# Optimization experiments

Hardware: AMD Instinct MI355X
Metric: run time of the kernel (lower is better)

Reference implementation:

```python
import jax, jax.numpy as jnp
import numpy as np

B, S, D = 1, 2048, 1024
NH, NKV, WS = 8, 2, 64
HD = D // NH  # 128
E, HDIM, TOPK = 16, 512, 2
FP16_MIN = -65504.0
EPS = 1e-6
AUX_COEFF = 1e-5


def rmsnorm(x, w):
    return x * jax.lax.rsqrt(jnp.mean(x * x, axis=-1, keepdims=True) + EPS) * w


def setup_inputs() -> dict:
    key = jax.random.key(0)
    ks = jax.random.split(key, 24)
    r = lambda k, shape, fan: jax.random.normal(k, shape, dtype=jnp.float32) * (1.0 / np.sqrt(fan))
    return {
        "x": jax.random.normal(ks[0], (B, S, D), dtype=jnp.float32),
        "norm1_w": jnp.ones((D,), jnp.float32),
        "wq": r(ks[1], (D, NH * HD), D), "bq": jnp.zeros((NH * HD,), jnp.float32),
        "wk": r(ks[2], (D, NKV * HD), D), "bk": jnp.zeros((NKV * HD,), jnp.float32),
        "wv": r(ks[3], (D, NKV * HD), D), "bv": jnp.zeros((NKV * HD,), jnp.float32),
        "wo": r(ks[4], (NH * HD, D), NH * HD), "bo": jnp.zeros((D,), jnp.float32),
        "sink_bias": jnp.zeros((), jnp.float32),
        "norm2_w": jnp.ones((D,), jnp.float32),
        "router_w": r(ks[5], (D, E), D), "router_b": jnp.zeros((E,), jnp.float32),
        "w1": r(ks[6], (E, D, HDIM), D), "b1": jnp.zeros((E, HDIM), jnp.float32),
        "w2": r(ks[7], (E, HDIM, D), HDIM), "b2": jnp.zeros((E, D), jnp.float32),
    }


def reference(x, norm1_w, wq, bq, wk, bk, wv, bv, wo, bo, sink_bias,
              norm2_w, router_w, router_b, w1, b1, w2, b2):
    # ---- sliding-window attention with sink softmax ----
    h = rmsnorm(x, norm1_w)
    q = (h @ wq + bq).reshape(B, S, NH, HD).transpose(0, 2, 1, 3)    # [B,NH,S,HD]
    k = (h @ wk + bk).reshape(B, S, NKV, HD).transpose(0, 2, 1, 3)   # [B,NKV,S,HD]
    v = (h @ wv + bv).reshape(B, S, NKV, HD).transpose(0, 2, 1, 3)
    k = jnp.repeat(k, NH // NKV, axis=1)  # GQA expand -> [B,NH,S,HD]
    v = jnp.repeat(v, NH // NKV, axis=1)
    scores = jnp.einsum('bhqd,bhkd->bhqk', q, k) / np.sqrt(HD)
    i = jnp.arange(S)[:, None]
    j = jnp.arange(S)[None, :]
    band = (i - j >= 0) & (i - j <= WS - 1)  # causal sliding window
    scores = jnp.where(band, scores, FP16_MIN)
    m = jnp.maximum(jnp.max(scores, axis=-1, keepdims=True), sink_bias)
    ew = jnp.exp(scores - m)
    denom = jnp.sum(ew, axis=-1, keepdims=True) + jnp.exp(sink_bias - m)
    attn = ew / denom
    out = jnp.einsum('bhqk,bhkd->bhqd', attn, v).transpose(0, 2, 1, 3).reshape(B, S, D)
    x = x + (out @ wo + bo)

    # ---- MoE FFN ----
    h2 = rmsnorm(x, norm2_w)
    xf = h2.reshape(-1, D)                                  # [N,D]
    logits = (xf @ router_w + router_b) / 0.1               # [N,E]
    top_v, top_i = jax.lax.top_k(logits, TOPK)              # [N,k]
    top_w = jax.nn.softmax(top_v, axis=-1)
    probs = jax.nn.softmax(logits, axis=-1)
    aux_loss = jnp.sum(jnp.sum(probs, axis=0) ** 2) / E * AUX_COEFF
    # combine weights per (token, expert)
    gate = jnp.sum(jax.nn.one_hot(top_i, E, dtype=xf.dtype) * top_w[..., None], axis=1)  # [N,E]
    hmid = jax.nn.silu(jnp.einsum('nd,edh->neh', xf, w1) + b1)   # [N,E,H]
    y = jnp.einsum('neh,ehd->ned', hmid, w2) + b2                # [N,E,D]
    ffn = jnp.einsum('ne,ned->nd', gate, y)
    x = x + ffn.reshape(B, S, D)
    return x, aux_loss
```

## Files before the change

kernel.cpp:

```cpp
#include <hip/hip_runtime.h>
#include <hip/hip_bf16.h>

#define S     2048
#define D     1024
#define NH    8
#define NKV   2
#define HD    128
#define WS_   64
#define E_    16
#define HDIM  512
#define TOPK  2
#define NTOK  S
#define NSLOT (S*TOPK)
#define QKV_M (D + 2*NKV*HD)
#define KOFF  D
#define VOFF  (D + NKV*HD)
#define QB    8
#define WROWS (QB + WS_ - 1)
#define KPITCH 73
#define VPADF  132

typedef __attribute__((ext_vector_type(8))) short bf16x8;
typedef __attribute__((ext_vector_type(4))) float floatx4;

__device__ inline short f2bf(float f) {
    __hip_bfloat16 b = __float2bfloat16(f);
    return *reinterpret_cast<short*>(&b);
}

__global__ __launch_bounds__(256) void tconv_all(
    const float* __restrict__ wq, const float* __restrict__ wk,
    const float* __restrict__ wv, const float* __restrict__ wo,
    const float* __restrict__ w1, const float* __restrict__ w2,
    const float* __restrict__ bq, const float* __restrict__ bk,
    const float* __restrict__ bv, const float* __restrict__ router_w,
    short* __restrict__ wqkvT, short* __restrict__ woT,
    short* __restrict__ w1T, short* __restrict__ w2T,
    float* __restrict__ bqkv, float* __restrict__ rwT,
    const float* __restrict__ x, const float* __restrict__ norm1_w,
    short* __restrict__ h_bf, float* __restrict__ gcsum,
    int* __restrict__ ghist)
{
    int id = blockIdx.x;
    if (id >= 18983) {
        int row = id - 18983, t = threadIdx.x;
        float4 v = ((const float4*)(x + (size_t)row * D))[t];
        float ss = v.x*v.x + v.y*v.y + v.z*v.z + v.w*v.w;
        #pragma unroll
        for (int off = 32; off; off >>= 1) ss += __shfl_xor(ss, off, 64);
        __shared__ float red[4];
        if ((t & 63) == 0) red[t >> 6] = ss;
        __syncthreads();
        float total = red[0] + red[1] + red[2] + red[3];
        float scale = rsqrtf(total * (1.0f / (float)D) + 1e-6f);
        float4 wv4 = ((const float4*)norm1_w)[t];
        short4 ob;
        ob.x = f2bf(v.x * scale * wv4.x); ob.y = f2bf(v.y * scale * wv4.y);
        ob.z = f2bf(v.z * scale * wv4.z); ob.w = f2bf(v.w * scale * wv4.w);
        ((short4*)(h_bf + (size_t)row * D))[t] = ob;
        return;
    }
    if (id == 18982) {
        int t = threadIdx.x;
        if (t < E_) gcsum[t] = 0.f;
        else if (t < 2 * E_) ghist[t - E_] = 0;
        return;
    }
    if (id >= 18950) {
        int ky = id - 18950;
        int t = threadIdx.x;
        int r = t >> 4, c = t & 15;
        int k0 = ky * 32;
        rwT[c * D + k0 + r]      = router_w[(k0 + r) * E_ + c];
        rwT[c * D + k0 + r + 16] = router_w[(k0 + r + 16) * E_ + c];
        return;
    }
    if (id >= 18944) {
        int t = (id - 18944) * 256 + threadIdx.x;
        if (t < D) bqkv[t] = bq[t];
        else if (t < VOFF) bqkv[t] = bk[t - D];
        else bqkv[t] = bv[t - VOFF];
        return;
    }
    const float* in; short* outp; int K, M, mx, ky;
    if (id < 1024)      { in = wq; outp = wqkvT;                  K = D; M = D;   int l = id;        mx = l & 31; ky = l >> 5; }
    else if (id < 1280) { in = wk; outp = wqkvT + (size_t)KOFF*D; K = D; M = 256; int l = id - 1024; mx = l & 7;  ky = l >> 3; }
    else if (id < 1536) { in = wv; outp = wqkvT + (size_t)VOFF*D; K = D; M = 256; int l = id - 1280; mx = l & 7;  ky = l >> 3; }
    else if (id < 2560) { in = wo; outp = woT;                    K = D; M = D;   int l = id - 1536; mx = l & 31; ky = l >> 5; }
    else if (id < 10752){ int l = id - 2560;  int e = l >> 9; int r = l & 511;
                          in = w1 + (size_t)e * D * HDIM; outp = w1T + (size_t)e * D * HDIM;
                          K = D; M = HDIM; mx = r & 15; ky = r >> 4; }
    else                { int l = id - 10752; int e = l >> 9; int r = l & 511;
                          in = w2 + (size_t)e * D * HDIM; outp = w2T + (size_t)e * D * HDIM;
                          K = HDIM; M = D; mx = r & 31; ky = r >> 5; }
    __shared__ float tile[32][33];
    int t = threadIdx.x, r = t >> 3, c4 = (t & 7) * 4;
    int k0 = ky * 32, m0 = mx * 32;
    float4 v = *(const float4*)&in[(size_t)(k0 + r) * M + m0 + c4];
    tile[r][c4 + 0] = v.x; tile[r][c4 + 1] = v.y;
    tile[r][c4 + 2] = v.z; tile[r][c4 + 3] = v.w;
    __syncthreads();
    short4 o;
    o.x = f2bf(tile[c4 + 0][r]);
    o.y = f2bf(tile[c4 + 1][r]);
    o.z = f2bf(tile[c4 + 2][r]);
    o.w = f2bf(tile[c4 + 3][r]);
    *(short4*)&outp[(size_t)(m0 + r) * K + k0 + c4] = o;
}

#define BT   64
#define BKS  64
#define BUFS (BT * BKS)

__device__ inline void gld16(const short* g, short* l) {
    __builtin_amdgcn_global_load_lds(
        (const __attribute__((address_space(1))) unsigned int*)g,
        (__attribute__((address_space(3))) unsigned int*)l, 16, 0, 0);
}

template <int V>
__global__ __launch_bounds__(256) void mgemm(
    const short* __restrict__ A, const short* __restrict__ Bt,
    const float* __restrict__ bias, float* __restrict__ C,
    short* __restrict__ Cb, const float* __restrict__ res, int K, int M,
    const int* __restrict__ offs, const float* __restrict__ tok_gate,
    const int* __restrict__ tok_map)
{
    int e = (V >= 2) ? blockIdx.z : 0;
    const short* Bte = (V >= 2) ? Bt + (size_t)e * M * K : Bt;
    const float* be  = (V >= 2) ? bias + (size_t)e * M : bias;

    int row_lo, row_hi;
    if (V >= 2) {
        row_lo = offs[e] + blockIdx.y * BT;
        row_hi = offs[e + 1];
        if (row_lo >= row_hi) return;
    } else {
        row_lo = blockIdx.y * BT;
        row_hi = 1 << 30;
    }
    int col0 = blockIdx.x * BT;

    __shared__ __align__(16) short As[3 * BUFS];
    __shared__ __align__(16) short Bs[3 * BUFS];

    int t = threadIdx.x;
    int wave = t >> 6, lane = t & 63;
    int lrow   = lane >> 3;
    int schunk = (lane & 7) ^ lrow;

    const short* aQ[2];
    const short* bQ[2];
    #pragma unroll
    for (int q = 0; q < 2; ++q) {
        int row = q * 32 + wave * 8 + lrow;
        int gr = row_lo + row;
        if (V >= 2 && gr >= row_hi) gr = row_lo;
        const short* arow;
        if (V == 2) arow = A + (size_t)(tok_map[gr] & (NTOK - 1)) * K;
        else        arow = A + (size_t)gr * K;
        aQ[q] = arow + (schunk << 3);
        bQ[q] = Bte + (size_t)(col0 + row) * K + (schunk << 3);
    }

    int rin = lane & 15, quad = lane >> 4;
    int wm = (wave & 1) * 32, wn = (wave >> 1) * 32;

    int cg0 = col0 + wn + rin;
    int cg1 = cg0 + 16;
    float bj[2] = { be[cg0], be[cg1] };
    float resv[2][2][4];
    if (V == 1) {
        #pragma unroll
        for (int i = 0; i < 2; ++i)
            #pragma unroll
            for (int j = 0; j < 2; ++j)
                #pragma unroll
                for (int rr = 0; rr < 4; ++rr)
                    resv[i][j][rr] = res[(size_t)(row_lo + wm + i*16 + quad*4 + rr) * M
                                         + (j ? cg1 : cg0)];
    }
    int   tmv[2][4];
    float tgv[2][4];
    if (V == 3) {
        #pragma unroll
        for (int i = 0; i < 2; ++i)
            #pragma unroll
            for (int rr = 0; rr < 4; ++rr) {
                int rg = row_lo + wm + i*16 + quad*4 + rr;
                tmv[i][rr] = tok_map[rg] & (NTOK - 1);
                tgv[i][rr] = tok_gate[rg];
            }
    }

    floatx4 acc[2][2];
    #pragma unroll
    for (int i = 0; i < 2; ++i)
        #pragma unroll
        for (int j = 0; j < 2; ++j)
            acc[i][j] = (floatx4){0.f, 0.f, 0.f, 0.f};

    const int NIT = K >> 6;

    #pragma unroll
    for (int q = 0; q < 2; ++q) {
        gld16(aQ[q], &As[(q * 32 + wave * 8) * BKS]);
        gld16(bQ[q], &Bs[(q * 32 + wave * 8) * BKS]);
    }
    if (NIT > 1) {
        #pragma unroll
        for (int q = 0; q < 2; ++q) {
            gld16(aQ[q] + 64, &As[BUFS + (q * 32 + wave * 8) * BKS]);
            gld16(bQ[q] + 64, &Bs[BUFS + (q * 32 + wave * 8) * BKS]);
        }
        asm volatile("s_waitcnt vmcnt(4)\n\ts_barrier" ::: "memory");
    } else {
        asm volatile("s_waitcnt vmcnt(0)\n\ts_barrier" ::: "memory");
    }
    __builtin_amdgcn_sched_barrier(0);

    int bread = 0;
    for (int it = 0; it < NIT; ++it) {
        if (it + 2 < NIT) {
            int bst = bread + 2; if (bst >= 3) bst -= 3;
            int kk = (it + 2) << 6;
            #pragma unroll
            for (int q = 0; q < 2; ++q) {
                gld16(aQ[q] + kk, &As[bst * BUFS + (q * 32 + wave * 8) * BKS]);
                gld16(bQ[q] + kk, &Bs[bst * BUFS + (q * 32 + wave * 8) * BKS]);
            }
        }
        const short* Ab = &As[bread * BUFS];
        const short* Bb = &Bs[bread * BUFS];
        #pragma unroll
        for (int s = 0; s < 2; ++s) {
            bf16x8 af[2], bfr[2];
            #pragma unroll
            for (int i = 0; i < 2; ++i) {
                int row = wm + i * 16 + rin;
                af[i] = *(const bf16x8*)&Ab[row * BKS
                        + ((((s << 2) | quad) ^ (rin & 7)) << 3)];
            }
            #pragma unroll
            for (int j = 0; j < 2; ++j) {
                int row = wn + j * 16 + rin;
                bfr[j] = *(const bf16x8*)&Bb[row * BKS
                        + ((((s << 2) | quad) ^ (rin & 7)) << 3)];
            }
            #pragma unroll
            for (int i = 0; i < 2; ++i)
                #pragma unroll
                for (int j = 0; j < 2; ++j)
                    acc[i][j] = __builtin_amdgcn_mfma_f32_16x16x32_bf16(
                        af[i], bfr[j], acc[i][j], 0, 0, 0);
        }
        if (it + 1 < NIT) {
            if (it + 2 < NIT)
                asm volatile("s_waitcnt vmcnt(4)\n\ts_barrier" ::: "memory");
            else
                asm volatile("s_waitcnt vmcnt(0)\n\ts_barrier" ::: "memory");
            __builtin_amdgcn_sched_barrier(0);
        }
        bread = bread + 1; if (bread >= 3) bread = 0;
    }

    #pragma unroll
    for (int i = 0; i < 2; ++i) {
        #pragma unroll
        for (int j = 0; j < 2; ++j) {
            int cg = j ? cg1 : cg0;
            #pragma unroll
            for (int rr = 0; rr < 4; ++rr) {
                int rg = row_lo + wm + i * 16 + quad * 4 + rr;
                float val = acc[i][j][rr];
                if (V == 0) {
                    C[(size_t)rg * M + cg] = val + bj[j];
                } else if (V == 1) {
                    C[(size_t)rg * M + cg] = val + bj[j] + resv[i][j][rr];
                } else if (V == 2) {
                    if (rg < row_hi) {
                        float vb_ = val + bj[j];
                        Cb[(size_t)rg * M + cg] = f2bf(vb_ / (1.f + __expf(-vb_)));
                    }
                } else {
                    if (rg < row_hi)
                        unsafeAtomicAdd(&C[(size_t)tmv[i][rr] * M + cg],
                                        tgv[i][rr] * (val + bj[j]));
                }
            }
        }
    }
}

__global__ __launch_bounds__(256) void attn_kernel(
    const float* __restrict__ qkv, const float* __restrict__ sink_ptr,
    short* __restrict__ ao)
{
    __shared__ __align__(16) float KT[32 * KPITCH * 4];
    __shared__ __align__(16) float Vs[WROWS * VPADF];
    __shared__ __align__(16) float Ps4[4][64][4];

    int qblk = blockIdx.x;
    int kvh  = blockIdx.y;
    int q0   = qblk * QB;
    int jbase = q0 - (WS_ - 1);

    int t = threadIdx.x;
    int c4 = (t & 31) * 4, c4g = t & 31;
    for (int r = t >> 5; r < WROWS; r += 8) {
        int j = jbase + r;
        float4 kv4 = make_float4(0.f, 0.f, 0.f, 0.f);
        float4 vv4 = make_float4(0.f, 0.f, 0.f, 0.f);
        if (j >= 0) {
            kv4 = *(const float4*)(qkv + (size_t)j * QKV_M + KOFF + kvh * HD + c4);
            vv4 = *(const float4*)(qkv + (size_t)j * QKV_M + VOFF + kvh * HD + c4);
        }
        *(float4*)&KT[(c4g * KPITCH + r) * 4] = kv4;
        *(float4*)&Vs[r * VPADF + c4] = vv4;
    }
    __syncthreads();

    int lane = t & 63, wv = t >> 6;
    float sink = sink_ptr[0];
    const float rscale = 0.08838834764831845f;

    #pragma unroll
    for (int g = 0; g < 2; ++g) {
        int qi = wv * 2 + g;
        int i  = q0 + qi;
        bool valid = (jbase + qi + lane) >= 0;

        float sc[4] = {0.f, 0.f, 0.f, 0.f};
        const float* qbase = qkv + (size_t)i * QKV_M + (kvh * 4) * HD;
        #pragma unroll
        for (int c = 0; c < 32; ++c) {
            float4 kx = *(const float4*)&KT[(c * KPITCH + qi + lane) * 4];
            #pragma unroll
            for (int hh = 0; hh < 4; ++hh) {
                float4 q4 = *(const float4*)(qbase + hh * HD + c * 4);
                sc[hh] += q4.x*kx.x + q4.y*kx.y + q4.z*kx.z + q4.w*kx.w;
            }
        }

        float pn[4];
        #pragma unroll
        for (int hh = 0; hh < 4; ++hh) {
            float s = valid ? sc[hh] * rscale : -1e30f;
            float m = s;
            #pragma unroll
            for (int off = 32; off; off >>= 1) m = fmaxf(m, __shfl_xor(m, off, 64));
            float mf = fmaxf(m, sink);
            float p  = __expf(s - mf);
            float ds = p;
            #pragma unroll
            for (int off = 32; off; off >>= 1) ds += __shfl_xor(ds, off, 64);
            pn[hh] = p / (ds + __expf(sink - mf));
        }
        *(float4*)&Ps4[wv][lane][0] = make_float4(pn[0], pn[1], pn[2], pn[3]);

        float o0=0,o1=0,o2=0,o3=0,o4=0,o5=0,o6=0,o7=0;
        const float* vp = &Vs[qi * VPADF + 2 * lane];
        #pragma unroll
        for (int jj = 0; jj < 64; ++jj) {
            float4 p4 = *(const float4*)&Ps4[wv][jj][0];
            float2 vv = *(const float2*)(vp + jj * VPADF);
            o0 += p4.x * vv.x; o1 += p4.x * vv.y;
            o2 += p4.y * vv.x; o3 += p4.y * vv.y;
            o4 += p4.z * vv.x; o5 += p4.z * vv.y;
            o6 += p4.w * vv.x; o7 += p4.w * vv.y;
        }
        short2 r0; r0.x = f2bf(o0); r0.y = f2bf(o1);
        short2 r1; r1.x = f2bf(o2); r1.y = f2bf(o3);
        short2 r2; r2.x = f2bf(o4); r2.y = f2bf(o5);
        short2 r3; r3.x = f2bf(o6); r3.y = f2bf(o7);
        ((short2*)(ao + (size_t)i * D + (kvh * 4 + 0) * HD))[lane] = r0;
        ((short2*)(ao + (size_t)i * D + (kvh * 4 + 1) * HD))[lane] = r1;
        ((short2*)(ao + (size_t)i * D + (kvh * 4 + 2) * HD))[lane] = r2;
        ((short2*)(ao + (size_t)i * D + (kvh * 4 + 3) * HD))[lane] = r3;
    }
}

__global__ __launch_bounds__(256) void rms_router_kernel(
    const float* __restrict__ x1, const float* __restrict__ w,
    short* __restrict__ h2b, const float* __restrict__ rwT,
    const float* __restrict__ rb, float* __restrict__ gcsum,
    int* __restrict__ ghist, int* __restrict__ top_i,
    float* __restrict__ top_g, float* __restrict__ out)
{
    int tok = blockIdx.x, t = threadIdx.x;
    __shared__ float hrow[D];
    float4 v = ((const float4*)(x1 + (size_t)tok * D))[t];
    ((float4*)(out + (size_t)tok * D))[t] = v;
    float ss = v.x*v.x + v.y*v.y + v.z*v.z + v.w*v.w;
    #pragma unroll
    for (int off = 32; off; off >>= 1) ss += __shfl_xor(ss, off, 64);
    __shared__ float red[4];
    if ((t & 63) == 0) red[t >> 6] = ss;
    __syncthreads();
    float total = red[0] + red[1] + red[2] + red[3];
    float scale = rsqrtf(total * (1.0f / (float)D) + 1e-6f);
    float4 wv = ((const float4*)w)[t];
    float4 o;
    o.x = v.x * scale * wv.x; o.y = v.y * scale * wv.y;
    o.z = v.z * scale * wv.z; o.w = v.w * scale * wv.w;
    ((float4*)hrow)[t] = o;
    short4 ob;
    ob.x = f2bf(o.x); ob.y = f2bf(o.y); ob.z = f2bf(o.z); ob.w = f2bf(o.w);
    ((short4*)(h2b + (size_t)tok * D))[t] = ob;
    __syncthreads();

    int e = t & 15, seg = t >> 4;
    const float4* rwp = (const float4*)(rwT + (size_t)e * D + seg * 64);
    const float4* hp  = (const float4*)(hrow + seg * 64);
    float part = 0.f;
    #pragma unroll
    for (int i = 0; i < 16; ++i) {
        float4 a = hp[i];
        float4 b = rwp[i];
        part += a.x * b.x; part += a.y * b.y;
        part += a.z * b.z; part += a.w * b.w;
    }
    __shared__ float lpart[256];
    lpart[t] = part;
    __syncthreads();
    __shared__ float logits[E_];
    if (t < E_) {
        float sl = 0.f;
        for (int sg = 0; sg < 16; ++sg) sl += lpart[sg * 16 + t];
        logits[t] = (sl + rb[t]) * 10.0f;
    }
    __syncthreads();
    __shared__ float sm[2];
    if (t == 0) {
        float mx = logits[0];
        for (int x_ = 1; x_ < E_; ++x_) mx = fmaxf(mx, logits[x_]);
        float ps = 0.f;
        for (int x_ = 0; x_ < E_; ++x_) ps += __expf(logits[x_] - mx);
        sm[0] = mx; sm[1] = ps;
        int i0 = 0; float v0 = logits[0];
        for (int x_ = 1; x_ < E_; ++x_) if (logits[x_] > v0) { v0 = logits[x_]; i0 = x_; }
        int i1 = (i0 == 0) ? 1 : 0; float v1 = logits[i1];
        for (int x_ = 0; x_ < E_; ++x_) {
            if (x_ == i0) continue;
            if (logits[x_] > v1) { v1 = logits[x_]; i1 = x_; }
        }
        float e1 = __expf(v1 - v0);
        float g0 = 1.f / (1.f + e1);
        float g1 = e1 * g0;
        top_i[tok * 2 + 0] = i0; top_g[tok * 2 + 0] = g0;
        top_i[tok * 2 + 1] = i1; top_g[tok * 2 + 1] = g1;
        atomicAdd(&ghist[i0], 1);
        atomicAdd(&ghist[i1], 1);
    }
    __syncthreads();
    if (t < E_)
        unsafeAtomicAdd(&gcsum[t], __expf(logits[t] - sm[0]) / sm[1]);
}

__global__ __launch_bounds__(256) void finalize_scatter_kernel(
    const float* __restrict__ gcsum, const int* __restrict__ ghist,
    const int* __restrict__ top_i, const float* __restrict__ top_g,
    int* __restrict__ offs, int* __restrict__ tok_idx,
    float* __restrict__ tok_gate, int* __restrict__ slot_of,
    float* __restrict__ aux_out)
{
    __shared__ int curs[E_];
    int t = threadIdx.x;
    if (t == 0) {
        int acc = 0;
        for (int e = 0; e < E_; ++e) { offs[e] = acc; curs[e] = acc; acc += ghist[e]; }
        offs[E_] = acc;
        float s = 0.f;
        for (int e = 0; e < E_; ++e) { float c = gcsum[e]; s += c * c; }
        *aux_out = s / (float)E_ * 1e-5f;
    }
    __syncthreads();

    for (int i = 0; i < NTOK / 256; ++i) {
        int tok = i * 256 + t;
        #pragma unroll
        for (int s = 0; s < TOPK; ++s) {
            int e = top_i[tok * 2 + s] & 15;
            int pos = atomicAdd(&curs[e], 1) & (NSLOT - 1);
            tok_idx[pos]  = tok;
            tok_gate[pos] = top_g[tok * 2 + s];
            slot_of[tok * 2 + s] = pos;
        }
    }
}

extern "C" void kernel_launch(void* const* d_in, const int* in_sizes, int n_in,
                              void* d_out, int out_size, void* d_ws, size_t ws_size,
                              hipStream_t stream)
{
    const float* x        = (const float*)d_in[0];
    const float* norm1_w  = (const float*)d_in[1];
    const float* wq       = (const float*)d_in[2];
    const float* bq       = (const float*)d_in[3];
    const float* wk       = (const float*)d_in[4];
    const float* bk       = (const float*)d_in[5];
    const float* wv       = (const float*)d_in[6];
    const float* bv       = (const float*)d_in[7];
    const float* wo       = (const float*)d_in[8];
    const float* bo       = (const float*)d_in[9];
    const float* sink     = (const float*)d_in[10];
    const float* norm2_w  = (const float*)d_in[11];
    const float* router_w = (const float*)d_in[12];
    const float* router_b = (const float*)d_in[13];
    const float* w1       = (const float*)d_in[14];
    const float* b1       = (const float*)d_in[15];
    const float* w2       = (const float*)d_in[16];
    const float* b2       = (const float*)d_in[17];
    float* out = (float*)d_out;

    char* w = (char*)d_ws;
    auto alloc = [&](size_t bytes) {
        char* p = w; w += (bytes + 255) & ~255ull; return p;
    };
    short* wqkvT = (short*)alloc((size_t)QKV_M * D * 2);
    short* woT   = (short*)alloc((size_t)D * D * 2);
    short* w1T   = (short*)alloc((size_t)E_ * HDIM * D * 2);
    short* w2T   = (short*)alloc((size_t)E_ * D * HDIM * 2);
    float* bqkv  = (float*)alloc(QKV_M * 4);
    float* rwT   = (float*)alloc((size_t)E_ * D * 4);
    short* h_bf  = (short*)alloc((size_t)S * D * 2);
    float* qkv   = (float*)alloc((size_t)S * QKV_M * 4);
    float* x1    = (float*)alloc((size_t)S * D * 4);
    short* h2b   = (short*)alloc((size_t)S * D * 2);
    float* gcsum = (float*)alloc(E_ * 4);
    int*   ghist = (int*)alloc(E_ * 4);
    int*   offs     = (int*)alloc(17 * 4);
    int*   top_i    = (int*)alloc((size_t)NSLOT * 4);
    float* top_g    = (float*)alloc((size_t)NSLOT * 4);
    int*   tok_idx  = (int*)alloc((size_t)NSLOT * 4);
    float* tok_gate = (float*)alloc((size_t)NSLOT * 4);
    int*   slot_of  = (int*)alloc((size_t)NSLOT * 4);
    short* ao_bf = h_bf;
    short* hmid  = (short*)qkv;

    tconv_all<<<21031, 256, 0, stream>>>(wq, wk, wv, wo, w1, w2, bq, bk, bv,
                                         router_w, wqkvT, woT, w1T, w2T,
                                         bqkv, rwT, x, norm1_w, h_bf,
                                         gcsum, ghist);

    mgemm<0><<<dim3(QKV_M / BT, S / BT), 256, 0, stream>>>(
        h_bf, wqkvT, bqkv, qkv, nullptr, nullptr, D, QKV_M, nullptr, nullptr,
        nullptr);

    attn_kernel<<<dim3(S / QB, NKV), 256, 0, stream>>>(qkv, sink, ao_bf);

    mgemm<1><<<dim3(D / BT, S / BT), 256, 0, stream>>>(
        ao_bf, woT, bo, x1, nullptr, x, D, D, nullptr, nullptr, nullptr);

    rms_router_kernel<<<NTOK, 256, 0, stream>>>(x1, norm2_w, h2b, rwT,
                                                router_b, gcsum, ghist,
                                                top_i, top_g, out);

    finalize_scatter_kernel<<<1, 256, 0, stream>>>(
        gcsum, ghist, top_i, top_g, offs, tok_idx, tok_gate, slot_of,
        out + (size_t)S * D);

    mgemm<2><<<dim3(HDIM / BT, NSLOT / BT, E_), 256, 0, stream>>>(
        h2b, w1T, b1, nullptr, hmid, nullptr, D, HDIM, offs, nullptr, tok_idx);

    mgemm<3><<<dim3(D / BT, NSLOT / BT, E_), 256, 0, stream>>>(
        hmid, w2T, b2, out, nullptr, nullptr, HDIM, D, offs, tok_gate, tok_idx);
}
```

Measured before the change: 306.6 us.

## Replace global router atomics with per-token probs buffer and in-block reduction

The router kernel now computes top-2 and the softmax with 16-lane shuffles instead of a serial single-thread loop, and writes per-token probabilities instead of doing global atomic adds for the expert histogram and the probability column sums. The single-block finalize kernel then reduces probs and top_i with shared-memory atomics, which removes the zero-init block and the global atomic contention. The cost is an extra 128KB probs buffer and a serial read of it by one block in finalize.

```diff
diff --git a/kernel.cpp b/kernel.cpp
--- a/kernel.cpp
+++ b/kernel.cpp
@@ -38,12 +38,11 @@
     short* __restrict__ w1T, short* __restrict__ w2T,
     float* __restrict__ bqkv, float* __restrict__ rwT,
     const float* __restrict__ x, const float* __restrict__ norm1_w,
-    short* __restrict__ h_bf, float* __restrict__ gcsum,
-    int* __restrict__ ghist)
+    short* __restrict__ h_bf)
 {
     int id = blockIdx.x;
-    if (id >= 18983) {
-        int row = id - 18983, t = threadIdx.x;
+    if (id >= 18982) {
+        int row = id - 18982, t = threadIdx.x;
         float4 v = ((const float4*)(x + (size_t)row * D))[t];
         float ss = v.x*v.x + v.y*v.y + v.z*v.z + v.w*v.w;
         #pragma unroll
@@ -58,12 +57,6 @@
         ob.x = f2bf(v.x * scale * wv4.x); ob.y = f2bf(v.y * scale * wv4.y);
         ob.z = f2bf(v.z * scale * wv4.z); ob.w = f2bf(v.w * scale * wv4.w);
         ((short4*)(h_bf + (size_t)row * D))[t] = ob;
-        return;
-    }
-    if (id == 18982) {
-        int t = threadIdx.x;
-        if (t < E_) gcsum[t] = 0.f;
-        else if (t < 2 * E_) ghist[t - E_] = 0;
         return;
     }
     if (id >= 18950) {
@@ -383,9 +376,9 @@
 __global__ __launch_bounds__(256) void rms_router_kernel(
     const float* __restrict__ x1, const float* __restrict__ w,
     short* __restrict__ h2b, const float* __restrict__ rwT,
-    const float* __restrict__ rb, float* __restrict__ gcsum,
-    int* __restrict__ ghist, int* __restrict__ top_i,
-    float* __restrict__ top_g, float* __restrict__ out)
+    const float* __restrict__ rb, float* __restrict__ probs,
+    int* __restrict__ top_i, float* __restrict__ top_g,
+    float* __restrict__ out)
 {
     int tok = blockIdx.x, t = threadIdx.x;
     __shared__ float hrow[D];
@@ -423,55 +416,73 @@
     __shared__ float lpart[256];
     lpart[t] = part;
     __syncthreads();
-    __shared__ float logits[E_];
+
     if (t < E_) {
         float sl = 0.f;
+        #pragma unroll
         for (int sg = 0; sg < 16; ++sg) sl += lpart[sg * 16 + t];
-        logits[t] = (sl + rb[t]) * 10.0f;
-    }
-    __syncthreads();
-    __shared__ float sm[2];
-    if (t == 0) {
-        float mx = logits[0];
-        for (int x_ = 1; x_ < E_; ++x_) mx = fmaxf(mx, logits[x_]);
-        float ps = 0.f;
-        for (int x_ = 0; x_ < E_; ++x_) ps += __expf(logits[x_] - mx);
-        sm[0] = mx; sm[1] = ps;
-        int i0 = 0; float v0 = logits[0];
-        for (int x_ = 1; x_ < E_; ++x_) if (logits[x_] > v0) { v0 = logits[x_]; i0 = x_; }
-        int i1 = (i0 == 0) ? 1 : 0; float v1 = logits[i1];
-        for (int x_ = 0; x_ < E_; ++x_) {
-            if (x_ == i0) continue;
-            if (logits[x_] > v1) { v1 = logits[x_]; i1 = x_; }
-        }
-        float e1 = __expf(v1 - v0);
-        float g0 = 1.f / (1.f + e1);
-        float g1 = e1 * g0;
-        top_i[tok * 2 + 0] = i0; top_g[tok * 2 + 0] = g0;
-        top_i[tok * 2 + 1] = i1; top_g[tok * 2 + 1] = g1;
-        atomicAdd(&ghist[i0], 1);
-        atomicAdd(&ghist[i1], 1);
-    }
-    __syncthreads();
-    if (t < E_)
-        unsafeAtomicAdd(&gcsum[t], __expf(logits[t] - sm[0]) / sm[1]);
+        float lv = (sl + rb[t]) * 10.0f;
+
+        float bv = lv; int bi = t;
+        #pragma unroll
+        for (int off = 8; off; off >>= 1) {
+            float ov = __shfl_xor(bv, off, 16);
+            int   oi = __shfl_xor(bi, off, 16);
+            if (ov > bv || (ov == bv && oi < bi)) { bv = ov; bi = oi; }
+        }
+        float lv2 = (t == bi) ? -3.402823e38f : lv;
+        float bv2 = lv2; int bi2 = t;
+        #pragma unroll
+        for (int off = 8; off; off >>= 1) {
+            float ov = __shfl_xor(bv2, off, 16);
+            int   oi = __shfl_xor(bi2, off, 16);
+            if (ov > bv2 || (ov == bv2 && oi < bi2)) { bv2 = ov; bi2 = oi; }
+        }
+        float pexp = __expf(lv - bv);
+        float ps = pexp;
+        #pragma unroll
+        for (int off = 8; off; off >>= 1) ps += __shfl_xor(ps, off, 16);
+        probs[tok * E_ + t] = pexp / ps;
+        if (t == 0) {
+            float e1 = __expf(bv2 - bv);
+            float g0 = 1.f / (1.f + e1);
+            top_i[tok * 2 + 0] = bi;  top_g[tok * 2 + 0] = g0;
+            top_i[tok * 2 + 1] = bi2; top_g[tok * 2 + 1] = e1 * g0;
+        }
+    }
 }
 
 __global__ __launch_bounds__(256) void finalize_scatter_kernel(
-    const float* __restrict__ gcsum, const int* __restrict__ ghist,
-    const int* __restrict__ top_i, const float* __restrict__ top_g,
-    int* __restrict__ offs, int* __restrict__ tok_idx,
-    float* __restrict__ tok_gate, int* __restrict__ slot_of,
-    float* __restrict__ aux_out)
+    const float* __restrict__ probs, const int* __restrict__ top_i,
+    const float* __restrict__ top_g, int* __restrict__ offs,
+    int* __restrict__ tok_idx, float* __restrict__ tok_gate,
+    int* __restrict__ slot_of, float* __restrict__ aux_out)
 {
+    __shared__ float csum[E_];
+    __shared__ int hist[E_];
     __shared__ int curs[E_];
     int t = threadIdx.x;
+    if (t < E_) { csum[t] = 0.f; hist[t] = 0; }
+    __syncthreads();
+
+    int c = t & 15, g = t >> 4;
+    float part = 0.f;
+    for (int i = 0; i < NTOK / 16; ++i)
+        part += probs[(size_t)(i * 16 + g) * E_ + c];
+    atomicAdd(&csum[c], part);
+
+    for (int i = 0; i < NSLOT / 256; ++i) {
+        int eidx = top_i[i * 256 + t] & 15;
+        atomicAdd(&hist[eidx], 1);
+    }
+    __syncthreads();
+
     if (t == 0) {
         int acc = 0;
-        for (int e = 0; e < E_; ++e) { offs[e] = acc; curs[e] = acc; acc += ghist[e]; }
+        for (int e = 0; e < E_; ++e) { offs[e] = acc; curs[e] = acc; acc += hist[e]; }
         offs[E_] = acc;
         float s = 0.f;
-        for (int e = 0; e < E_; ++e) { float c = gcsum[e]; s += c * c; }
+        for (int e = 0; e < E_; ++e) s += csum[e] * csum[e];
         *aux_out = s / (float)E_ * 1e-5f;
     }
     __syncthreads();
@@ -527,8 +538,7 @@
     float* qkv   = (float*)alloc((size_t)S * QKV_M * 4);
     float* x1    = (float*)alloc((size_t)S * D * 4);
     short* h2b   = (short*)alloc((size_t)S * D * 2);
-    float* gcsum = (float*)alloc(E_ * 4);
-    int*   ghist = (int*)alloc(E_ * 4);
+    float* probs = (float*)alloc((size_t)NTOK * E_ * 4);
     int*   offs     = (int*)alloc(17 * 4);
     int*   top_i    = (int*)alloc((size_t)NSLOT * 4);
     float* top_g    = (float*)alloc((size_t)NSLOT * 4);
@@ -538,10 +548,9 @@
     short* ao_bf = h_bf;
     short* hmid  = (short*)qkv;
 
-    tconv_all<<<21031, 256, 0, stream>>>(wq, wk, wv, wo, w1, w2, bq, bk, bv,
+    tconv_all<<<21030, 256, 0, stream>>>(wq, wk, wv, wo, w1, w2, bq, bk, bv,
                                          router_w, wqkvT, woT, w1T, w2T,
-                                         bqkv, rwT, x, norm1_w, h_bf,
-                                         gcsum, ghist);
+                                         bqkv, rwT, x, norm1_w, h_bf);
 
     mgemm<0><<<dim3(QKV_M / BT, S / BT), 256, 0, stream>>>(
         h_bf, wqkvT, bqkv, qkv, nullptr, nullptr, D, QKV_M, nullptr, nullptr,
@@ -553,11 +562,11 @@
         ao_bf, woT, bo, x1, nullptr, x, D, D, nullptr, nullptr, nullptr);
 
     rms_router_kernel<<<NTOK, 256, 0, stream>>>(x1, norm2_w, h2b, rwT,
-                                                router_b, gcsum, ghist,
-                                                top_i, top_g, out);
+                                                router_b, probs, top_i, top_g,
+                                                out);
 
     finalize_scatter_kernel<<<1, 256, 0, stream>>>(
-        gcsum, ghist, top_i, top_g, offs, tok_idx, tok_gate, slot_of,
+        probs, top_i, top_g, offs, tok_idx, tok_gate, slot_of,
         out + (size_t)S * D);
 
     mgemm<2><<<dim3(HDIM / BT, NSLOT / BT, E_), 256, 0, stream>>>(
```

After: 275.5 us. -10.2%, faster.
